# Kernel optimization log

Hardware: AMD Instinct MI355X
Metric: run time of the kernel (lower is better)

The kernel has to match this reference:

```python
import jax, jax.numpy as jnp
import numpy as np

N_NODES = 100000
N_EDGES = 1600000
INPUT_DIM = 512
HIDDEN = 64
N_LAYERS = 3


def setup_inputs() -> dict:
    key = jax.random.key(0)
    ks = jax.random.split(key, 8)
    s = 0.05
    return {
        "x": jax.random.normal(ks[0], (N_NODES, INPUT_DIM), jnp.float32),
        "edge_index": jax.random.randint(ks[1], (2, N_EDGES), 0, N_NODES, jnp.int64),
        "W_enc": jax.random.normal(ks[2], (INPUT_DIM, HIDDEN), jnp.float32) * s,
        "b_enc": jnp.zeros((HIDDEN,), jnp.float32),
        "Wl": jax.random.normal(ks[3], (N_LAYERS, HIDDEN, HIDDEN), jnp.float32) * s,
        "bl": jnp.zeros((N_LAYERS, HIDDEN), jnp.float32),
        "Wr": jax.random.normal(ks[4], (N_LAYERS, HIDDEN, HIDDEN), jnp.float32) * s,
        "W_cls": jax.random.normal(ks[5], (HIDDEN, 1), jnp.float32) * s,
        "b_cls": jnp.zeros((1,), jnp.float32),
    }


def reference(x, edge_index, W_enc, b_enc, Wl, bl, Wr, W_cls, b_cls):
    # node encoder
    h = x @ W_enc + b_enc  # [N, H]
    N = h.shape[0]
    src, dst = edge_index[0], edge_index[1]  # messages flow src -> dst (PyG convention)
    ones = jnp.ones((src.shape[0],), h.dtype)
    deg = jax.ops.segment_sum(ones, dst, num_segments=N)  # in-degree per node
    inv_deg = jnp.where(deg > 0, 1.0 / jnp.maximum(deg, 1.0), 0.0)[:, None]
    n_layers = Wl.shape[0]
    for l in range(n_layers):
        # SAGEConv: mean-aggregate neighbor features, transform, add root transform
        msgs = h[src]  # [E, H] gather
        agg = jax.ops.segment_sum(msgs, dst, num_segments=N) * inv_deg  # mean aggr
        h_new = agg @ Wl[l] + bl[l] + h @ Wr[l]
        h = jax.nn.relu(h + h_new)  # residual + relu
    out = jax.nn.sigmoid(h @ W_cls + b_cls)  # [N, 1]
    return out.squeeze(-1)
```

## Files before the change

### kernel.cpp

```cpp
#include <hip/hip_runtime.h>
#include <math.h>

#define HID 64
#define KIN 512
#define NBK_MAX 256

typedef __attribute__((ext_vector_type(8))) short short8;
typedef __attribute__((ext_vector_type(4))) float floatx4;
typedef __attribute__((ext_vector_type(2))) float floatx2;

__device__ inline unsigned bf16pair(float a, float b) {
  unsigned ua = __float_as_uint(a);
  unsigned ub = __float_as_uint(b);
  ua = (ua + 0x7FFFu + ((ua >> 16) & 1u)) >> 16;
  ub = (ub + 0x7FFFu + ((ub >> 16) & 1u)) >> 16;
  return ua | (ub << 16);
}
__device__ inline unsigned short bf16one(float a) {
  unsigned ua = __float_as_uint(a);
  return (unsigned short)((ua + 0x7FFFu + ((ua >> 16) & 1u)) >> 16);
}
__device__ inline unsigned char fp8q(float a) {
  const int pk = __builtin_amdgcn_cvt_pk_fp8_f32(a, a, 0, false);
  return (unsigned char)(pk & 0xff);
}

__global__ __launch_bounds__(1024) void prep_bucket_kernel(
    const float* __restrict__ We, const float* __restrict__ Wl,
    const float* __restrict__ Wr, unsigned short* __restrict__ wte,
    unsigned short* __restrict__ wlrt, const int* __restrict__ src,
    const int* __restrict__ dst, int* __restrict__ cnt,
    int* __restrict__ gcur, unsigned* __restrict__ ebuf, int E, int N,
    int NBK, int CAP) {
  const int blk = blockIdx.x;
  const int tid = threadIdx.x;
  if (blk < 32) {
    const int t = blk * 1024 + tid;
    const int c = t >> 9, k = t & 511;
    wte[c * KIN + k] = bf16one(We[k * HID + c]);
    return;
  }
  if (blk < 56) {
    const int t = (blk - 32) * 1024 + tid;
    if (t < 24576) {
      const int mat = t >> 12;
      const int e = t & 4095;
      const int c = e >> 6, k = e & 63;
      const float* sp = (mat < 3) ? (Wl + (size_t)mat * 4096)
                                  : (Wr + (size_t)(mat - 3) * 4096);
      wlrt[(size_t)mat * 4096 + c * 64 + k] = bf16one(sp[k * 64 + c]);
    }
    return;
  }
  __shared__ int hist[NBK_MAX];
  __shared__ int bbase[NBK_MAX];
  __shared__ int curloc[NBK_MAX];
  const int e0 = (blk - 56) * 4096;
  for (int i = tid; i < NBK; i += 1024) {
    hist[i] = 0;
    curloc[i] = 0;
  }
  __syncthreads();
  int bk[4];
  unsigned pk[4];
#pragma unroll
  for (int u = 0; u < 4; u++) {
    const int e = e0 + u * 1024 + tid;
    bk[u] = -1;
    pk[u] = 0;
    if (e < E) {
      const int d = dst[e];
      if ((unsigned)d < (unsigned)N) {
        int s = src[e];
        if ((unsigned)s >= (unsigned)N) s = 0;
        bk[u] = d >> 9;
        pk[u] = ((unsigned)s << 9) | (unsigned)(d & 511);
        atomicAdd(&hist[bk[u]], 1);
        atomicAdd(&cnt[d], 1);
      }
    }
  }
  __syncthreads();
  for (int i = tid; i < NBK; i += 1024)
    if (hist[i]) bbase[i] = atomicAdd(&gcur[i], hist[i]);
  __syncthreads();
#pragma unroll
  for (int u = 0; u < 4; u++) {
    if (bk[u] >= 0) {
      const int gp = bbase[bk[u]] + atomicAdd(&curloc[bk[u]], 1);
      if (gp < CAP) ebuf[(size_t)bk[u] * CAP + gp] = pk[u];
    }
  }
}

__global__ __launch_bounds__(1024) void scanA_kernel(
    const int* __restrict__ cnt, int* __restrict__ block_sums, int N) {
  __shared__ int red[1024];
  const int tid = threadIdx.x;
  const int i = blockIdx.x * 1024 + tid;
  red[tid] = (i < N) ? cnt[i] : 0;
  __syncthreads();
  for (int off = 512; off > 0; off >>= 1) {
    if (tid < off) red[tid] += red[tid + off];
    __syncthreads();
  }
  if (tid == 0) block_sums[blockIdx.x] = red[0];
}

__global__ __launch_bounds__(1024) void scanC_kernel(
    const int* __restrict__ cnt, const int* __restrict__ block_sums,
    int* __restrict__ row_start, float* __restrict__ inv_deg, int N) {
  __shared__ int part[1024];
  __shared__ int soff;
  const int tid = threadIdx.x;
  const int i = blockIdx.x * 1024 + tid;
  if (tid < 64) {
    int s = 0;
    for (int b2 = tid; b2 < blockIdx.x; b2 += 64) s += block_sums[b2];
#pragma unroll
    for (int off = 32; off > 0; off >>= 1) s += __shfl_down(s, off, 64);
    if (tid == 0) soff = s;
  }
  const int v = (i < N) ? cnt[i] : 0;
  part[tid] = v;
  __syncthreads();
  for (int off = 1; off < 1024; off <<= 1) {
    int t = (tid >= off) ? part[tid - off] : 0;
    __syncthreads();
    part[tid] += t;
    __syncthreads();
  }
  if (i < N) {
    row_start[i] = soff + part[tid] - v;
    inv_deg[i] = (v > 0) ? 1.0f / (float)v : 0.0f;
  }
  if (blockIdx.x == gridDim.x - 1 && tid == 1023)
    row_start[N] = soff + part[1023];
}

__global__ __launch_bounds__(256) void scatter_enc_kernel(
    const unsigned* __restrict__ ebuf, const int* __restrict__ gcur,
    const int* __restrict__ row_start, int* __restrict__ csr_src,
    const float* __restrict__ x, const unsigned short* __restrict__ wt,
    const float* __restrict__ b, unsigned short* __restrict__ hb,
    unsigned char* __restrict__ h8, int N, int NBK, int CAP) {
  __shared__ uint4 sx[2][256];
  __shared__ uint4 sw[2][256];
  __shared__ int cur[512];
  __shared__ int rsl[512];
  if (blockIdx.x < (unsigned)NBK) {
    const int bkt = blockIdx.x;
    const int nodeBase = bkt << 9;
    const int tid = threadIdx.x;
    cur[tid] = 0;
    cur[tid + 256] = 0;
    rsl[tid] = (nodeBase + tid < N) ? row_start[nodeBase + tid] : 0;
    rsl[tid + 256] =
        (nodeBase + tid + 256 < N) ? row_start[nodeBase + tid + 256] : 0;
    __syncthreads();
    int cnt_b = gcur[bkt];
    if (cnt_b > CAP) cnt_b = CAP;
    const unsigned* eb = ebuf + (size_t)bkt * CAP;
    for (int i = tid; i < cnt_b; i += 256) {
      const unsigned p = eb[i];
      const int dl = p & 511;
      const int pos = rsl[dl] + atomicAdd(&cur[dl], 1);
      csr_src[pos] = (int)(p >> 9);
    }
    return;
  }
  const int t = threadIdx.x;
  const int lane = t & 63;
  const int wid = t >> 6;
  const int m15 = lane & 15;
  const int quad = lane >> 4;
  const int blockBase = (blockIdx.x - NBK) * 64;

  const int rs = t >> 2;
  const int qs = t & 3;
  const int us = rs * 4 + (qs ^ ((rs >> 1) & 3));
  const int gn = blockBase + rs;
  const bool valid = gn < N;
  const float* xp = x + (size_t)(valid ? gn : 0) * KIN + qs * 8;
  const unsigned short* wp = wt + (size_t)rs * KIN + qs * 8;

  const int arow = wid * 16 + m15;
  const int ua = arow * 4 + (quad ^ ((arow >> 1) & 3));
  int ub[4];
#pragma unroll
  for (int c4 = 0; c4 < 4; c4++) {
    const int col = c4 * 16 + m15;
    ub[c4] = col * 4 + (quad ^ ((col >> 1) & 3));
  }

  floatx4 acc[4];
#pragma unroll
  for (int c4 = 0; c4 < 4; c4++)
#pragma unroll
    for (int j = 0; j < 4; j++) acc[c4][j] = 0.f;

  float4 fx0, fx1;
  uint4 wv;
  if (valid) {
    fx0 = *(const float4*)(xp);
    fx1 = *(const float4*)(xp + 4);
  } else {
    fx0 = fx1 = make_float4(0.f, 0.f, 0.f, 0.f);
  }
  wv = *(const uint4*)(wp);

  for (int kc = 0; kc < 16; kc++) {
    const int curb = kc & 1;
    uint4 xu;
    xu.x = bf16pair(fx0.x, fx0.y);
    xu.y = bf16pair(fx0.z, fx0.w);
    xu.z = bf16pair(fx1.x, fx1.y);
    xu.w = bf16pair(fx1.z, fx1.w);
    sx[curb][us] = xu;
    sw[curb][us] = wv;
    __syncthreads();
    if (kc < 15) {
      const int ko = (kc + 1) * 32;
      if (valid) {
        fx0 = *(const float4*)(xp + ko);
        fx1 = *(const float4*)(xp + ko + 4);
      }
      wv = *(const uint4*)(wp + ko);
    }
    const short8 a = __builtin_bit_cast(short8, sx[curb][ua]);
#pragma unroll
    for (int c4 = 0; c4 < 4; c4++) {
      const short8 bf = __builtin_bit_cast(short8, sw[curb][ub[c4]]);
      acc[c4] =
          __builtin_amdgcn_mfma_f32_16x16x32_bf16(a, bf, acc[c4], 0, 0, 0);
    }
  }

#pragma unroll
  for (int c4 = 0; c4 < 4; c4++) {
    const float bias = b[c4 * 16 + m15];
#pragma unroll
    for (int r = 0; r < 4; r++) {
      const int row = blockBase + wid * 16 + quad * 4 + r;
      if (row < N) {
        const float v = acc[c4][r] + bias;
        hb[(size_t)row * HID + c4 * 16 + m15] = bf16one(v);
        h8[(size_t)row * HID + c4 * 16 + m15] = fp8q(v);
      }
    }
  }
}

__global__ __launch_bounds__(256) void layer_kernel(
    const unsigned short* __restrict__ hin,
    const unsigned char* __restrict__ h8in, unsigned short* __restrict__ hout,
    unsigned char* __restrict__ h8out, const int* __restrict__ row_start,
    const int* __restrict__ csr_src, const float* __restrict__ inv_deg,
    const unsigned short* __restrict__ Wlt,
    const unsigned short* __restrict__ Wrt, const float* __restrict__ bl,
    const float* __restrict__ Wc, const float* __restrict__ bc,
    float* __restrict__ out, int N) {
  __shared__ uint4 sAgg[512];
  __shared__ uint4 sH[512];
  __shared__ uint4 sWl[512];
  __shared__ uint4 sWr[512];
  const int tid = threadIdx.x;
  const int lane = tid & 63;
  const int wid = tid >> 6;
  const int m15 = lane & 15;
  const int quad = lane >> 4;
  const int blockBase = blockIdx.x * 64;

  {
    const int r = tid >> 2;
    const int gp = tid & 3;
    const int g0 = gp * 2, g1 = gp * 2 + 1;
    const int u0 = r * 8 + (g0 ^ (r & 7));
    const int u1 = r * 8 + (g1 ^ (r & 7));
    const int gn = blockBase + r;
    if (gn < N) {
      const uint4* hp = (const uint4*)(hin + (size_t)gn * HID);
      sH[u0] = hp[g0];
      sH[u1] = hp[g1];
    } else {
      const uint4 z = make_uint4(0, 0, 0, 0);
      sH[u0] = z;
      sH[u1] = z;
    }
    const uint4* wl = (const uint4*)(Wlt + (size_t)r * HID);
    const uint4* wr = (const uint4*)(Wrt + (size_t)r * HID);
    sWl[u0] = wl[g0];
    sWl[u1] = wl[g1];
    sWr[u0] = wr[g0];
    sWr[u1] = wr[g1];
  }

  {
    const int slot = lane >> 2;
    const int qc = lane & 3;
    const int nl = wid * 16 + slot;
    const int gn = blockBase + nl;
    float a[16];
#pragma unroll
    for (int c = 0; c < 16; c++) a[c] = 0.f;
    float id = 0.f;
    if (gn < N) {
      id = inv_deg[gn];
      const int s = row_start[gn];
      const int e = row_start[gn + 1];
      for (int j = s; j < e; j += 8) {
        int n[8];
        bool ok[8];
#pragma unroll
        for (int u = 0; u < 8; u++) {
          const int jj = j + u;
          ok[u] = jj < e;
          n[u] = csr_src[ok[u] ? jj : j];
        }
        uint4 v[8];
#pragma unroll
        for (int u = 0; u < 8; u++) {
          v[u] = *(const uint4*)(h8in + (size_t)n[u] * HID + qc * 16);
        }
#pragma unroll
        for (int u = 0; u < 8; u++) {
          if (!ok[u]) v[u] = make_uint4(0, 0, 0, 0);
#if __has_builtin(__builtin_amdgcn_cvt_pk_f32_fp8)
          {
            floatx2 p;
            p = __builtin_amdgcn_cvt_pk_f32_fp8((int)v[u].x, false);
            a[0] += p[0]; a[1] += p[1];
            p = __builtin_amdgcn_cvt_pk_f32_fp8((int)v[u].x, true);
            a[2] += p[0]; a[3] += p[1];
            p = __builtin_amdgcn_cvt_pk_f32_fp8((int)v[u].y, false);
            a[4] += p[0]; a[5] += p[1];
            p = __builtin_amdgcn_cvt_pk_f32_fp8((int)v[u].y, true);
            a[6] += p[0]; a[7] += p[1];
            p = __builtin_amdgcn_cvt_pk_f32_fp8((int)v[u].z, false);
            a[8] += p[0]; a[9] += p[1];
            p = __builtin_amdgcn_cvt_pk_f32_fp8((int)v[u].z, true);
            a[10] += p[0]; a[11] += p[1];
            p = __builtin_amdgcn_cvt_pk_f32_fp8((int)v[u].w, false);
            a[12] += p[0]; a[13] += p[1];
            p = __builtin_amdgcn_cvt_pk_f32_fp8((int)v[u].w, true);
            a[14] += p[0]; a[15] += p[1];
          }
#else
          a[0] += __builtin_amdgcn_cvt_f32_fp8(v[u].x, 0);
          a[1] += __builtin_amdgcn_cvt_f32_fp8(v[u].x, 1);
          a[2] += __builtin_amdgcn_cvt_f32_fp8(v[u].x, 2);
          a[3] += __builtin_amdgcn_cvt_f32_fp8(v[u].x, 3);
          a[4] += __builtin_amdgcn_cvt_f32_fp8(v[u].y, 0);
          a[5] += __builtin_amdgcn_cvt_f32_fp8(v[u].y, 1);
          a[6] += __builtin_amdgcn_cvt_f32_fp8(v[u].y, 2);
          a[7] += __builtin_amdgcn_cvt_f32_fp8(v[u].y, 3);
          a[8] += __builtin_amdgcn_cvt_f32_fp8(v[u].z, 0);
          a[9] += __builtin_amdgcn_cvt_f32_fp8(v[u].z, 1);
          a[10] += __builtin_amdgcn_cvt_f32_fp8(v[u].z, 2);
          a[11] += __builtin_amdgcn_cvt_f32_fp8(v[u].z, 3);
          a[12] += __builtin_amdgcn_cvt_f32_fp8(v[u].w, 0);
          a[13] += __builtin_amdgcn_cvt_f32_fp8(v[u].w, 1);
          a[14] += __builtin_amdgcn_cvt_f32_fp8(v[u].w, 2);
          a[15] += __builtin_amdgcn_cvt_f32_fp8(v[u].w, 3);
#endif
        }
      }
    }
    uint4 p0, p1;
    p0.x = bf16pair(a[0] * id, a[1] * id);
    p0.y = bf16pair(a[2] * id, a[3] * id);
    p0.z = bf16pair(a[4] * id, a[5] * id);
    p0.w = bf16pair(a[6] * id, a[7] * id);
    p1.x = bf16pair(a[8] * id, a[9] * id);
    p1.y = bf16pair(a[10] * id, a[11] * id);
    p1.z = bf16pair(a[12] * id, a[13] * id);
    p1.w = bf16pair(a[14] * id, a[15] * id);
    sAgg[nl * 8 + ((qc * 2) ^ (nl & 7))] = p0;
    sAgg[nl * 8 + ((qc * 2 + 1) ^ (nl & 7))] = p1;
  }
  __syncthreads();

  floatx4 acc[4];
#pragma unroll
  for (int c4 = 0; c4 < 4; c4++)
#pragma unroll
    for (int j = 0; j < 4; j++) acc[c4][j] = 0.f;

  const int arow = wid * 16 + m15;
#pragma unroll
  for (int c = 0; c < 2; c++) {
    const int ua = arow * 8 + ((c * 4 + quad) ^ (arow & 7));
    const short8 aA = __builtin_bit_cast(short8, sAgg[ua]);
    const short8 aH = __builtin_bit_cast(short8, sH[ua]);
#pragma unroll
    for (int c4 = 0; c4 < 4; c4++) {
      const int col = c4 * 16 + m15;
      const int ub = col * 8 + ((c * 4 + quad) ^ (col & 7));
      acc[c4] = __builtin_amdgcn_mfma_f32_16x16x32_bf16(
          aA, __builtin_bit_cast(short8, sWl[ub]), acc[c4], 0, 0, 0);
      acc[c4] = __builtin_amdgcn_mfma_f32_16x16x32_bf16(
          aH, __builtin_bit_cast(short8, sWr[ub]), acc[c4], 0, 0, 0);
    }
  }

  float vals[4][4];
#pragma unroll
  for (int c4 = 0; c4 < 4; c4++) {
    const float bias = bl[c4 * 16 + m15];
#pragma unroll
    for (int r = 0; r < 4; r++) {
      const int rowl = wid * 16 + quad * 4 + r;
      const unsigned short hv =
          ((const unsigned short*)
               sH)[(rowl * 8 + ((c4 * 2 + (m15 >> 3)) ^ (rowl & 7))) * 8 +
                   (m15 & 7)];
      const float v = __uint_as_float((unsigned)hv << 16) + acc[c4][r] + bias;
      vals[c4][r] = v > 0.f ? v : 0.f;
    }
  }
#pragma unroll
  for (int c4 = 0; c4 < 4; c4++) {
#pragma unroll
    for (int r = 0; r < 4; r++) {
      const int rowg = blockBase + wid * 16 + quad * 4 + r;
      if (rowg < N)
        hout[(size_t)rowg * HID + c4 * 16 + m15] = bf16one(vals[c4][r]);
    }
  }
  if (h8out != nullptr) {
#pragma unroll
    for (int c4 = 0; c4 < 4; c4++) {
#pragma unroll
      for (int r = 0; r < 4; r++) {
        const int rowg = blockBase + wid * 16 + quad * 4 + r;
        if (rowg < N)
          h8out[(size_t)rowg * HID + c4 * 16 + m15] = fp8q(vals[c4][r]);
      }
    }
  }
  if (Wc != nullptr) {
    float p[4] = {0.f, 0.f, 0.f, 0.f};
#pragma unroll
    for (int c4 = 0; c4 < 4; c4++) {
      const float wc = Wc[c4 * 16 + m15];
#pragma unroll
      for (int r = 0; r < 4; r++) p[r] += vals[c4][r] * wc;
    }
#pragma unroll
    for (int off = 1; off < 16; off <<= 1) {
#pragma unroll
      for (int r = 0; r < 4; r++) p[r] += __shfl_xor(p[r], off, 16);
    }
    if (m15 == 0) {
      const float bb = bc[0];
#pragma unroll
      for (int r = 0; r < 4; r++) {
        const int rowg = blockBase + wid * 16 + quad * 4 + r;
        if (rowg < N) out[rowg] = 1.0f / (1.0f + expf(-(p[r] + bb)));
      }
    }
  }
}

extern "C" void kernel_launch(void* const* d_in, const int* in_sizes, int n_in,
                              void* d_out, int out_size, void* d_ws,
                              size_t ws_size, hipStream_t stream) {
  const float* x = (const float*)d_in[0];
  const int* ei = (const int*)d_in[1];
  const float* W_enc = (const float*)d_in[2];
  const float* b_enc = (const float*)d_in[3];
  const float* Wl = (const float*)d_in[4];
  const float* bl = (const float*)d_in[5];
  const float* Wr = (const float*)d_in[6];
  const float* Wc = (const float*)d_in[7];
  const float* bc = (const float*)d_in[8];
  float* out = (float*)d_out;

  const int N = in_sizes[0] / KIN;
  const int E = in_sizes[1] / 2;
  const int* src = ei;
  const int* dst = ei + E;

  const int NBK = (N + 511) >> 9;
  int CAP = E / (NBK > 0 ? NBK : 1);
  CAP = CAP + (CAP >> 1) + 1024;
  CAP = (CAP + 255) & ~255;

  char* ws = (char*)d_ws;
  size_t off = 0;
  auto alloc = [&](size_t bytes) -> void* {
    void* p = ws + off;
    off += (bytes + 255) & ~(size_t)255;
    return p;
  };
  unsigned short* hb0 =
      (unsigned short*)alloc((size_t)N * HID * sizeof(unsigned short));
  unsigned short* hb1 =
      (unsigned short*)alloc((size_t)N * HID * sizeof(unsigned short));
  unsigned char* h8a = (unsigned char*)alloc((size_t)N * HID);
  unsigned char* h8b = (unsigned char*)alloc((size_t)N * HID);
  int* cnt = (int*)alloc((size_t)N * sizeof(int));
  int* gcur = (int*)alloc((size_t)NBK * sizeof(int));
  int* row_start = (int*)alloc((size_t)(N + 1) * sizeof(int));
  float* inv_deg = (float*)alloc((size_t)N * sizeof(float));
  int* csr_src = (int*)alloc((size_t)E * sizeof(int));
  unsigned* ebuf = (unsigned*)alloc((size_t)NBK * CAP * sizeof(unsigned));
  const int nblk = (N + 1023) / 1024;
  int* block_sums = (int*)alloc((size_t)nblk * sizeof(int));
  unsigned short* wte =
      (unsigned short*)alloc((size_t)HID * KIN * sizeof(unsigned short));
  unsigned short* wlrt =
      (unsigned short*)alloc((size_t)6 * HID * HID * sizeof(unsigned short));

  hipMemsetAsync(cnt, 0, (size_t)N * sizeof(int), stream);
  hipMemsetAsync(gcur, 0, (size_t)NBK * sizeof(int), stream);

  const int nbktA = (E + 4095) / 4096;
  prep_bucket_kernel<<<56 + nbktA, 1024, 0, stream>>>(
      W_enc, Wl, Wr, wte, wlrt, src, dst, cnt, gcur, ebuf, E, N, NBK, CAP);
  scanA_kernel<<<nblk, 1024, 0, stream>>>(cnt, block_sums, N);
  scanC_kernel<<<nblk, 1024, 0, stream>>>(cnt, block_sums, row_start, inv_deg,
                                          N);
  const int nb64 = (N + 63) / 64;
  scatter_enc_kernel<<<NBK + nb64, 256, 0, stream>>>(
      ebuf, gcur, row_start, csr_src, x, wte, b_enc, hb0, h8a, N, NBK, CAP);

  layer_kernel<<<nb64, 256, 0, stream>>>(hb0, h8a, hb1, h8b, row_start, csr_src,
                                         inv_deg, wlrt, wlrt + 3 * 4096, bl,
                                         nullptr, nullptr, nullptr, N);
  layer_kernel<<<nb64, 256, 0, stream>>>(hb1, h8b, hb0, h8a, row_start, csr_src,
                                         inv_deg, wlrt + 4096, wlrt + 4 * 4096,
                                         bl + 64, nullptr, nullptr, nullptr, N);
  layer_kernel<<<nb64, 256, 0, stream>>>(hb0, h8a, hb1, nullptr, row_start,
                                         csr_src, inv_deg, wlrt + 2 * 4096,
                                         wlrt + 5 * 4096, bl + 128, Wc, bc, out,
                                         N);
}
```

Baseline: 494.7 us.

## Compute per-node degrees and row offsets inside bucket scatter, drop scan kernels

Removes the global per-node atomic degree counter, the cnt memset and the two scan kernels. Each bucket block now builds a shared-memory degree histogram from its edge bucket, prefix-sums bucket totals from gcur for its global offset, and writes row_start and inv_deg before scattering into CSR. Shared memory is merged into one aliased buffer. This cuts 1.6M global atomics and two launches, but adds an extra pass over each bucket's edges and a serial prefix over preceding bucket counts.

```diff
diff --git a/kernel.cpp b/kernel.cpp
--- a/kernel.cpp
+++ b/kernel.cpp
@@ -29,9 +29,8 @@
     const float* __restrict__ We, const float* __restrict__ Wl,
     const float* __restrict__ Wr, unsigned short* __restrict__ wte,
     unsigned short* __restrict__ wlrt, const int* __restrict__ src,
-    const int* __restrict__ dst, int* __restrict__ cnt,
-    int* __restrict__ gcur, unsigned* __restrict__ ebuf, int E, int N,
-    int NBK, int CAP) {
+    const int* __restrict__ dst, int* __restrict__ gcur,
+    unsigned* __restrict__ ebuf, int E, int N, int NBK, int CAP) {
   const int blk = blockIdx.x;
   const int tid = threadIdx.x;
   if (blk < 32) {
@@ -76,7 +75,6 @@
         bk[u] = d >> 9;
         pk[u] = ((unsigned)s << 9) | (unsigned)(d & 511);
         atomicAdd(&hist[bk[u]], 1);
-        atomicAdd(&cnt[d], 1);
       }
     }
   }
@@ -93,74 +91,65 @@
   }
 }
 
-__global__ __launch_bounds__(1024) void scanA_kernel(
-    const int* __restrict__ cnt, int* __restrict__ block_sums, int N) {
-  __shared__ int red[1024];
-  const int tid = threadIdx.x;
-  const int i = blockIdx.x * 1024 + tid;
-  red[tid] = (i < N) ? cnt[i] : 0;
-  __syncthreads();
-  for (int off = 512; off > 0; off >>= 1) {
-    if (tid < off) red[tid] += red[tid + off];
-    __syncthreads();
-  }
-  if (tid == 0) block_sums[blockIdx.x] = red[0];
-}
-
-__global__ __launch_bounds__(1024) void scanC_kernel(
-    const int* __restrict__ cnt, const int* __restrict__ block_sums,
-    int* __restrict__ row_start, float* __restrict__ inv_deg, int N) {
-  __shared__ int part[1024];
-  __shared__ int soff;
-  const int tid = threadIdx.x;
-  const int i = blockIdx.x * 1024 + tid;
-  if (tid < 64) {
-    int s = 0;
-    for (int b2 = tid; b2 < blockIdx.x; b2 += 64) s += block_sums[b2];
-#pragma unroll
-    for (int off = 32; off > 0; off >>= 1) s += __shfl_down(s, off, 64);
-    if (tid == 0) soff = s;
-  }
-  const int v = (i < N) ? cnt[i] : 0;
-  part[tid] = v;
-  __syncthreads();
-  for (int off = 1; off < 1024; off <<= 1) {
-    int t = (tid >= off) ? part[tid - off] : 0;
-    __syncthreads();
-    part[tid] += t;
-    __syncthreads();
-  }
-  if (i < N) {
-    row_start[i] = soff + part[tid] - v;
-    inv_deg[i] = (v > 0) ? 1.0f / (float)v : 0.0f;
-  }
-  if (blockIdx.x == gridDim.x - 1 && tid == 1023)
-    row_start[N] = soff + part[1023];
-}
-
 __global__ __launch_bounds__(256) void scatter_enc_kernel(
     const unsigned* __restrict__ ebuf, const int* __restrict__ gcur,
-    const int* __restrict__ row_start, int* __restrict__ csr_src,
-    const float* __restrict__ x, const unsigned short* __restrict__ wt,
-    const float* __restrict__ b, unsigned short* __restrict__ hb,
-    unsigned char* __restrict__ h8, int N, int NBK, int CAP) {
-  __shared__ uint4 sx[2][256];
-  __shared__ uint4 sw[2][256];
-  __shared__ int cur[512];
-  __shared__ int rsl[512];
+    int* __restrict__ row_start, float* __restrict__ inv_deg,
+    int* __restrict__ csr_src, const float* __restrict__ x,
+    const unsigned short* __restrict__ wt, const float* __restrict__ b,
+    unsigned short* __restrict__ hb, unsigned char* __restrict__ h8, int N,
+    int NBK, int CAP) {
+  __shared__ __align__(16) unsigned char smem[16384];
   if (blockIdx.x < (unsigned)NBK) {
+    int* cur = (int*)smem;
+    int* rsl = (int*)(smem + 2048);
+    int* psc = (int*)(smem + 4096);
+    int* soffp = (int*)(smem + 5120);
     const int bkt = blockIdx.x;
     const int nodeBase = bkt << 9;
     const int tid = threadIdx.x;
     cur[tid] = 0;
     cur[tid + 256] = 0;
-    rsl[tid] = (nodeBase + tid < N) ? row_start[nodeBase + tid] : 0;
-    rsl[tid + 256] =
-        (nodeBase + tid + 256 < N) ? row_start[nodeBase + tid + 256] : 0;
     __syncthreads();
     int cnt_b = gcur[bkt];
     if (cnt_b > CAP) cnt_b = CAP;
     const unsigned* eb = ebuf + (size_t)bkt * CAP;
+    for (int i = tid; i < cnt_b; i += 256) atomicAdd(&cur[eb[i] & 511], 1);
+    if (tid < 64) {
+      int s = 0;
+      for (int b2 = tid; b2 < bkt; b2 += 64) s += gcur[b2];
+#pragma unroll
+      for (int off = 32; off > 0; off >>= 1) s += __shfl_down(s, off, 64);
+      if (tid == 0) *soffp = s;
+    }
+    __syncthreads();
+    const int d0 = cur[2 * tid];
+    const int d1 = cur[2 * tid + 1];
+    psc[tid] = d0 + d1;
+    __syncthreads();
+    for (int off = 1; off < 256; off <<= 1) {
+      int t = (tid >= off) ? psc[tid - off] : 0;
+      __syncthreads();
+      psc[tid] += t;
+      __syncthreads();
+    }
+    const int soff = *soffp;
+    const int base0 = soff + psc[tid] - (d0 + d1);
+    rsl[2 * tid] = base0;
+    rsl[2 * tid + 1] = base0 + d0;
+    const int g0 = nodeBase + 2 * tid;
+    const int g1 = g0 + 1;
+    if (g0 < N) {
+      row_start[g0] = base0;
+      inv_deg[g0] = d0 ? 1.0f / (float)d0 : 0.f;
+    }
+    if (g1 < N) {
+      row_start[g1] = base0 + d0;
+      inv_deg[g1] = d1 ? 1.0f / (float)d1 : 0.f;
+    }
+    if (bkt == NBK - 1 && tid == 255) row_start[N] = soff + psc[255];
+    cur[tid] = 0;
+    cur[tid + 256] = 0;
+    __syncthreads();
     for (int i = tid; i < cnt_b; i += 256) {
       const unsigned p = eb[i];
       const int dl = p & 511;
@@ -169,6 +158,8 @@
     }
     return;
   }
+  uint4(*sx)[256] = (uint4(*)[256])smem;
+  uint4(*sw)[256] = (uint4(*)[256])(smem + 8192);
   const int t = threadIdx.x;
   const int lane = t & 63;
   const int wid = t >> 6;
@@ -499,31 +490,25 @@
       (unsigned short*)alloc((size_t)N * HID * sizeof(unsigned short));
   unsigned char* h8a = (unsigned char*)alloc((size_t)N * HID);
   unsigned char* h8b = (unsigned char*)alloc((size_t)N * HID);
-  int* cnt = (int*)alloc((size_t)N * sizeof(int));
   int* gcur = (int*)alloc((size_t)NBK * sizeof(int));
   int* row_start = (int*)alloc((size_t)(N + 1) * sizeof(int));
   float* inv_deg = (float*)alloc((size_t)N * sizeof(float));
   int* csr_src = (int*)alloc((size_t)E * sizeof(int));
   unsigned* ebuf = (unsigned*)alloc((size_t)NBK * CAP * sizeof(unsigned));
-  const int nblk = (N + 1023) / 1024;
-  int* block_sums = (int*)alloc((size_t)nblk * sizeof(int));
   unsigned short* wte =
       (unsigned short*)alloc((size_t)HID * KIN * sizeof(unsigned short));
   unsigned short* wlrt =
       (unsigned short*)alloc((size_t)6 * HID * HID * sizeof(unsigned short));
 
-  hipMemsetAsync(cnt, 0, (size_t)N * sizeof(int), stream);
   hipMemsetAsync(gcur, 0, (size_t)NBK * sizeof(int), stream);
 
   const int nbktA = (E + 4095) / 4096;
   prep_bucket_kernel<<<56 + nbktA, 1024, 0, stream>>>(
-      W_enc, Wl, Wr, wte, wlrt, src, dst, cnt, gcur, ebuf, E, N, NBK, CAP);
-  scanA_kernel<<<nblk, 1024, 0, stream>>>(cnt, block_sums, N);
-  scanC_kernel<<<nblk, 1024, 0, stream>>>(cnt, block_sums, row_start, inv_deg,
-                                          N);
+      W_enc, Wl, Wr, wte, wlrt, src, dst, gcur, ebuf, E, N, NBK, CAP);
   const int nb64 = (N + 63) / 64;
   scatter_enc_kernel<<<NBK + nb64, 256, 0, stream>>>(
-      ebuf, gcur, row_start, csr_src, x, wte, b_enc, hb0, h8a, N, NBK, CAP);
+      ebuf, gcur, row_start, inv_deg, csr_src, x, wte, b_enc, hb0, h8a, N, NBK,
+      CAP);
 
   layer_kernel<<<nb64, 256, 0, stream>>>(hb0, h8a, hb1, h8b, row_start, csr_src,
                                          inv_deg, wlrt, wlrt + 3 * 4096, bl,
```

After: 431.5 us. -12.8%, faster.
